# Kernel optimization log

Measured on AMD Instinct MI355X. Metric: run time of the kernel, lower is better.

Reference implementation:

```python
import jax, jax.numpy as jnp
import numpy as np
from jax import lax

B, H, W, K = 32, 384, 384, 16
SENT = H * W          # sentinel label for background / padding
THRESH = 0.75


def setup_inputs() -> dict:
    key = jax.random.key(0)
    ks = jax.random.split(key, 20)
    s = 0.1
    def n(k, shp):
        return jax.random.normal(k, shp, jnp.float32) * s
    return {
        'x1': jax.random.normal(ks[0], (B, 1, H, W), jnp.float32),
        'x2': jax.random.normal(ks[1], (B, 1, H, W), jnp.float32),
        'e1_w': n(ks[2], (16, 1, 4, 4)), 'e1_b': n(ks[3], (16,)),
        'e2_w': n(ks[4], (32, 16, 4, 4)), 'e2_b': n(ks[5], (32,)),
        'e3_w': n(ks[6], (64, 32, 4, 4)), 'e3_b': n(ks[7], (64,)),
        'd3_w': n(ks[8], (64, 32, 4, 4)), 'd3_b': n(ks[9], (32,)),
        'd2_w': n(ks[10], (64, 16, 4, 4)), 'd2_b': n(ks[11], (16,)),
        'd1_w': n(ks[12], (32, 1, 4, 4)), 'd1_b': n(ks[13], (1,)),
        'w1': n(ks[14], (32, 32)), 'b1': n(ks[15], (32,)),
        'w2': n(ks[16], (8, 32)), 'b2': n(ks[17], (8,)),
        'w3': n(ks[18], (1, 8)), 'b3': n(ks[19], (1,)),
    }


def _conv(x, w, b):  # Conv2d(k=4, s=2, p=1), torch OIHW weights
    y = lax.conv_general_dilated(x, w, (2, 2), ((1, 1), (1, 1)),
                                 dimension_numbers=('NCHW', 'OIHW', 'NCHW'))
    return y + b[None, :, None, None]


def _convT(x, w, b):  # ConvTranspose2d(k=4, s=2, p=1), torch (in,out,kh,kw) weights
    wf = jnp.flip(w, (2, 3)).transpose(1, 0, 2, 3)  # -> OIHW
    y = lax.conv_general_dilated(x, wf, (1, 1), ((2, 2), (2, 2)), lhs_dilation=(2, 2),
                                 dimension_numbers=('NCHW', 'OIHW', 'NCHW'))
    return y + b[None, :, None, None]


def _autoencoder(x, e1_w, e1_b, e2_w, e2_b, e3_w, e3_b, d3_w, d3_b, d2_w, d2_b, d1_w, d1_b):
    x1 = jax.nn.relu(_conv(x, e1_w, e1_b))
    x2 = jax.nn.relu(_conv(x1, e2_w, e2_b))
    x3 = jax.nn.relu(_conv(x2, e3_w, e3_b))
    d3 = jax.nn.relu(_convT(x3, d3_w, d3_b))
    d3 = jnp.concatenate([d3, x2], axis=1)
    d2 = jax.nn.relu(_convT(d3, d2_w, d2_b))
    d2 = jnp.concatenate([d2, x1], axis=1)
    return jax.nn.sigmoid(_convT(d2, d1_w, d1_b))


def _extract(heat):
    # 8-connected components via iterative min-label propagation, then
    # centroid -> (radius, angle deg mod 360) around image center, sorted by radius.
    fg = heat > THRESH
    idx = jnp.arange(SENT, dtype=jnp.int32).reshape(H, W)
    l0 = jnp.where(fg, idx, SENT)

    def cond(c):
        return c[1]

    def body(c):
        l, _ = c
        pooled = lax.reduce_window(l, jnp.int32(SENT), lax.min, (3, 3), (1, 1), 'SAME')
        nl = jnp.where(fg, jnp.minimum(l, pooled), SENT)
        return nl, jnp.any(nl != l)

    labels, _ = lax.while_loop(cond, body, (l0, jnp.array(True)))
    flat = labels.ravel()
    u = jnp.unique(flat, size=K + 1, fill_value=SENT)[:K]  # up to K component roots
    valid = u < SENT
    n = valid.sum()
    mask = ((flat[None, :] == u[:, None]) & valid[:, None]).astype(jnp.float32)  # (K, HW)
    cnt = jnp.maximum(mask.sum(1), 1.0)
    cols = (jnp.arange(SENT) % W).astype(jnp.float32)
    rows = (jnp.arange(SENT) // W).astype(jnp.float32)
    cx = mask @ cols / cnt
    cy = mask @ rows / cnt
    dx = cx - (W // 2)
    dy = cy - (H // 2)
    r = jnp.sqrt(dx * dx + dy * dy)
    a = jnp.rad2deg(jnp.arctan2(dy, dx)) % 360.0
    order = jnp.argsort(jnp.where(valid, r, jnp.inf))
    r = jnp.where(valid, r, 0.0)[order]
    a = jnp.where(valid, a, 0.0)[order]
    return r, a, n


def _match(r1, a1, n1, r2, a2, n2):
    # greedy nearest-radius matching of the smaller set against the larger,
    # zero padding up to K pairs; diff = (r1-r2, |sin(radians(a1-a2))|)
    swap = n1 > n2
    rA = jnp.where(swap, r2, r1); aA = jnp.where(swap, a2, a1); nA = jnp.where(swap, n2, n1)
    rB = jnp.where(swap, r1, r2); aB = jnp.where(swap, a1, a2); nB = jnp.where(swap, n1, n2)
    iota = jnp.arange(K)

    def step(used, xs):
        i, rAi, aAi = xs
        vi = i < nA
        d = jnp.where(used | (iota >= nB), jnp.inf, jnp.abs(rB - rAi))
        j = jnp.argmin(d)
        dr = rAi - rB[j]
        da = jnp.abs(jnp.sin(jnp.deg2rad(aAi - aB[j])))
        out = jnp.where(vi, jnp.stack([dr, da]), 0.0)
        used = used.at[j].set(used[j] | vi)
        return used, out

    _, ys = lax.scan(step, jnp.zeros(K, bool), (iota, rA, aA))
    return ys.ravel()  # (2K,) interleaved (dr, da) like torch flatten


def _features(x1, x2, enc):
    h1 = _autoencoder(x1, *enc)[:, 0]  # (B,H,W)
    h2 = _autoencoder(x2, *enc)[:, 0]
    r1, a1, n1 = jax.vmap(_extract)(h1)
    r2, a2, n2 = jax.vmap(_extract)(h2)
    return jax.vmap(_match)(r1, a1, n1, r2, a2, n2)  # (B, 2K)


def reference(x1, x2, e1_w, e1_b, e2_w, e2_b, e3_w, e3_b, d3_w, d3_b, d2_w, d2_b, d1_w, d1_b, w1, b1, w2, b2, w3, b3):
    enc = (e1_w, e1_b, e2_w, e2_b, e3_w, e3_b, d3_w, d3_b, d2_w, d2_b, d1_w, d1_b)
    feats = _features(x1, x2, enc)
    h = jax.nn.relu(feats @ w1.T + b1)
    h = jax.nn.relu(h @ w2.T + b2)
    return (h @ w3.T + b3)[:, 0]
```

## Files before the change

kernel.cpp:

```cpp
#include <hip/hip_runtime.h>
#include <math.h>

#define NIMG 32
#define SENTI 147456
#define CAPR 36864
#define LBG 0x7FFFFFFF

__device__ __forceinline__ int uf_load(int* P, int i) {
  return __hip_atomic_load(&P[i], __ATOMIC_RELAXED, __HIP_MEMORY_SCOPE_AGENT);
}
__device__ int uf_find(int* P, int i) {
  int p = uf_load(P, i);
  while (p != i) {
    int gp = uf_load(P, p);
    if (gp != p) atomicMin(&P[i], gp);
    i = p; p = gp;
  }
  return i;
}
__device__ void uf_union(int* P, int a, int b) {
  while (true) {
    a = uf_find(P, a); b = uf_find(P, b);
    if (a == b) return;
    if (a > b) { int t = a; a = b; b = t; }
    int old = atomicMin(&P[b], a);
    if (old == b) return;
    b = old;
  }
}

__device__ __forceinline__ int l_load(int* lab, int i) {
  return __hip_atomic_load(&lab[i], __ATOMIC_RELAXED, __HIP_MEMORY_SCOPE_WORKGROUP);
}
__device__ int l_find(int* lab, int i) {
  int p = l_load(lab, i);
  while (p != i) { int gp = l_load(lab, p); i = p; p = gp; }
  return i;
}
__device__ void l_union(int* lab, int a, int b) {
  while (true) {
    a = l_find(lab, a); b = l_find(lab, b);
    if (a == b) return;
    if (a > b) { int t = a; a = b; b = t; }
    int old = atomicMin(&lab[b], a);
    if (old == b) return;
    b = old;
  }
}

__global__ __launch_bounds__(256) void k_conv_e1(
    const float* __restrict__ x, const float* __restrict__ w,
    const float* __restrict__ bias, float* __restrict__ out)
{
  int idx = blockIdx.x * 256 + threadIdx.x;
  int ox = idx % 192; int t = idx / 192; int oy = t % 192; int img = t / 192;
  const float* xi = x + (size_t)img * 147456;
  float acc[16];
#pragma unroll
  for (int c = 0; c < 16; c++) acc[c] = bias[c];
#pragma unroll
  for (int ky = 0; ky < 4; ky++) {
    int iy = 2 * oy + ky - 1;
    if (iy < 0 || iy >= 384) continue;
    const float* row = xi + iy * 384;
#pragma unroll
    for (int kx = 0; kx < 4; kx++) {
      int ix = 2 * ox + kx - 1;
      if (ix < 0 || ix >= 384) continue;
      float v = row[ix];
#pragma unroll
      for (int c = 0; c < 16; c++) acc[c] = fmaf(v, w[c * 16 + ky * 4 + kx], acc[c]);
    }
  }
  size_t base = (size_t)img * 589824 + (size_t)oy * 192 + ox;
#pragma unroll
  for (int c = 0; c < 16; c++) out[base + (size_t)c * 36864] = fmaxf(acc[c], 0.f);
}

__global__ __launch_bounds__(256) void k_conv_e2(
    const float* __restrict__ in, const float* __restrict__ w,
    const float* __restrict__ bias, float* __restrict__ out)
{
  int idx = blockIdx.x * 256 + threadIdx.x;
  int p = idx % 48; int t = idx / 48; int oy = t % 96; int img = t / 96;
  const float* xin = in + (size_t)img * 589824;
  float accA[32], accB[32];
#pragma unroll
  for (int c = 0; c < 32; c++) { float bv = bias[c]; accA[c] = bv; accB[c] = bv; }
#pragma unroll 1
  for (int ci = 0; ci < 16; ci++) {
    const float* xc = xin + (size_t)ci * 36864;
#pragma unroll
    for (int ky = 0; ky < 4; ky++) {
      int iy = 2 * oy + ky - 1;
      float xv[6];
      if (iy >= 0 && iy < 192) {
        const float* row = xc + iy * 192;
        int c0 = 4 * p - 1;
#pragma unroll
        for (int u = 0; u < 6; u++) {
          int ix = c0 + u;
          xv[u] = (ix >= 0 && ix < 192) ? row[ix] : 0.f;
        }
      } else {
#pragma unroll
        for (int u = 0; u < 6; u++) xv[u] = 0.f;
      }
#pragma unroll
      for (int co = 0; co < 32; co++) {
        float4 wv = *(const float4*)(w + ((size_t)co * 16 + ci) * 16 + ky * 4);
        accA[co] = fmaf(xv[3], wv.w, fmaf(xv[2], wv.z, fmaf(xv[1], wv.y, fmaf(xv[0], wv.x, accA[co]))));
        accB[co] = fmaf(xv[5], wv.w, fmaf(xv[4], wv.z, fmaf(xv[3], wv.y, fmaf(xv[2], wv.x, accB[co]))));
      }
    }
  }
  size_t base = (size_t)img * 294912 + (size_t)oy * 96 + 2 * p;
#pragma unroll
  for (int co = 0; co < 32; co++) {
    float2 v; v.x = fmaxf(accA[co], 0.f); v.y = fmaxf(accB[co], 0.f);
    *(float2*)(out + base + (size_t)co * 9216) = v;
  }
}

__global__ __launch_bounds__(256) void k_conv_e3(
    const float* __restrict__ in, const float* __restrict__ w,
    const float* __restrict__ bias, float* __restrict__ out)
{
  int idx = blockIdx.x * 256 + threadIdx.x;
  int cog = blockIdx.y;
  int p = idx % 24; int t = idx / 24; int oy = t % 48; int img = t / 48;
  const float* xin = in + (size_t)img * 294912;
  float accA[16], accB[16];
#pragma unroll
  for (int c = 0; c < 16; c++) { float bv = bias[cog * 16 + c]; accA[c] = bv; accB[c] = bv; }
#pragma unroll 1
  for (int ci = 0; ci < 32; ci++) {
    const float* xc = xin + (size_t)ci * 9216;
#pragma unroll
    for (int ky = 0; ky < 4; ky++) {
      int iy = 2 * oy + ky - 1;
      float xv[6];
      if (iy >= 0 && iy < 96) {
        const float* row = xc + iy * 96;
        int c0 = 4 * p - 1;
#pragma unroll
        for (int u = 0; u < 6; u++) {
          int ix = c0 + u;
          xv[u] = (ix >= 0 && ix < 96) ? row[ix] : 0.f;
        }
      } else {
#pragma unroll
        for (int u = 0; u < 6; u++) xv[u] = 0.f;
      }
#pragma unroll
      for (int co = 0; co < 16; co++) {
        float4 wv = *(const float4*)(w + ((size_t)(cog * 16 + co) * 32 + ci) * 16 + ky * 4);
        accA[co] = fmaf(xv[3], wv.w, fmaf(xv[2], wv.z, fmaf(xv[1], wv.y, fmaf(xv[0], wv.x, accA[co]))));
        accB[co] = fmaf(xv[5], wv.w, fmaf(xv[4], wv.z, fmaf(xv[3], wv.y, fmaf(xv[2], wv.x, accB[co]))));
      }
    }
  }
  size_t base = (size_t)img * 147456 + (size_t)(cog * 16) * 2304 + (size_t)oy * 48 + 2 * p;
#pragma unroll
  for (int co = 0; co < 16; co++) {
    float2 v; v.x = fmaxf(accA[co], 0.f); v.y = fmaxf(accB[co], 0.f);
    *(float2*)(out + base + (size_t)co * 2304) = v;
  }
}

__global__ __launch_bounds__(256) void k_convt_d3(
    const float* __restrict__ in, const float* __restrict__ w,
    const float* __restrict__ bias, float* __restrict__ out)
{
  int idx = blockIdx.x * 256 + threadIdx.x;
  int p = idx % 48; int t = idx / 48; int oy = t % 96; int img = t / 96;
  int iy1 = (oy + 1) >> 1; int iy0 = iy1 - 1;
  int ky1 = (oy + 1) - 2 * iy1; int ky0 = ky1 + 2;
  bool v1 = (iy1 < 48), v0 = (iy0 >= 0);
  bool pm = (p > 0), pp = (p < 47);
  float accA[32], accB[32];
#pragma unroll
  for (int c = 0; c < 32; c++) { float bv = bias[c]; accA[c] = bv; accB[c] = bv; }
#pragma unroll 1
  for (int ci = 0; ci < 64; ci++) {
    const float* xc = in + (size_t)img * 147456 + (size_t)ci * 2304;
    const float* r1 = xc + iy1 * 48; const float* r0 = xc + iy0 * 48;
    float x1m = (v1 && pm) ? r1[p - 1] : 0.f;
    float x1c = v1 ? r1[p] : 0.f;
    float x1p = (v1 && pp) ? r1[p + 1] : 0.f;
    float x0m = (v0 && pm) ? r0[p - 1] : 0.f;
    float x0c = v0 ? r0[p] : 0.f;
    float x0p = (v0 && pp) ? r0[p + 1] : 0.f;
    const float* wb = w + (size_t)ci * 512;
#pragma unroll
    for (int co = 0; co < 32; co++) {
      float4 wv1 = *(const float4*)(wb + co * 16 + ky1 * 4);
      float4 wv0 = *(const float4*)(wb + co * 16 + ky0 * 4);
      accA[co] += x1c * wv1.y + x1m * wv1.w + x0c * wv0.y + x0m * wv0.w;
      accB[co] += x1p * wv1.x + x1c * wv1.z + x0p * wv0.x + x0c * wv0.z;
    }
  }
  size_t base = (size_t)img * 294912 + (size_t)oy * 96 + 2 * p;
#pragma unroll
  for (int co = 0; co < 32; co++) {
    float2 v; v.x = fmaxf(accA[co], 0.f); v.y = fmaxf(accB[co], 0.f);
    *(float2*)(out + base + (size_t)co * 9216) = v;
  }
}

__global__ __launch_bounds__(256) void k_convt_d2(
    const float* __restrict__ d3, const float* __restrict__ e2,
    const float* __restrict__ w, const float* __restrict__ bias,
    float* __restrict__ out)
{
  int idx = blockIdx.x * 256 + threadIdx.x;
  int pg = idx % 24; int t = idx / 24; int oy = t % 192; int img = t / 192;
  int iy1 = (oy + 1) >> 1; int iy0 = iy1 - 1;
  int ky1 = (oy + 1) - 2 * iy1; int ky0 = ky1 + 2;
  bool v1 = (iy1 < 96), v0 = (iy0 >= 0);
  int c0 = 4 * pg - 1;
  float acc[16][8];
#pragma unroll
  for (int co = 0; co < 16; co++) {
    float bv = bias[co];
#pragma unroll
    for (int j = 0; j < 8; j++) acc[co][j] = bv;
  }
  for (int half = 0; half < 2; half++) {
    const float* src = (half == 0) ? d3 : e2;
#pragma unroll 1
    for (int ci = 0; ci < 32; ci++) {
      const float* xc = src + (size_t)img * 294912 + (size_t)ci * 9216;
      const float* r1 = xc + iy1 * 96; const float* r0 = xc + iy0 * 96;
      float x1[6], x0[6];
#pragma unroll
      for (int u = 0; u < 6; u++) {
        int ix = c0 + u;
        bool cb = (ix >= 0) && (ix < 96);
        x1[u] = (v1 && cb) ? r1[ix] : 0.f;
        x0[u] = (v0 && cb) ? r0[ix] : 0.f;
      }
      const float* wb = w + (size_t)(half * 32 + ci) * 256;
#pragma unroll
      for (int co = 0; co < 16; co++) {
        float4 wv1 = *(const float4*)(wb + co * 16 + ky1 * 4);
        float4 wv0 = *(const float4*)(wb + co * 16 + ky0 * 4);
#pragma unroll
        for (int j = 0; j < 4; j++) {
          acc[co][2 * j]     += x1[j + 1] * wv1.y + x1[j] * wv1.w
                              + x0[j + 1] * wv0.y + x0[j] * wv0.w;
          acc[co][2 * j + 1] += x1[j + 2] * wv1.x + x1[j + 1] * wv1.z
                              + x0[j + 2] * wv0.x + x0[j + 1] * wv0.z;
        }
      }
    }
  }
  size_t base = (size_t)img * 589824 + (size_t)oy * 192 + 8 * pg;
#pragma unroll
  for (int co = 0; co < 16; co++) {
    float4 a, b;
    a.x = fmaxf(acc[co][0], 0.f); a.y = fmaxf(acc[co][1], 0.f);
    a.z = fmaxf(acc[co][2], 0.f); a.w = fmaxf(acc[co][3], 0.f);
    b.x = fmaxf(acc[co][4], 0.f); b.y = fmaxf(acc[co][5], 0.f);
    b.z = fmaxf(acc[co][6], 0.f); b.w = fmaxf(acc[co][7], 0.f);
    *(float4*)(out + base + (size_t)co * 36864)     = a;
    *(float4*)(out + base + (size_t)co * 36864 + 4) = b;
  }
}

__global__ __launch_bounds__(256) void k_convt_d1(
    const float* __restrict__ d2, const float* __restrict__ e1,
    const float* __restrict__ w, const float* __restrict__ bias,
    int* __restrict__ parent)
{
  int idx = blockIdx.x * 256 + threadIdx.x;
  int p = idx % 192; int t = idx / 192; int oy = t % 384; int img = t / 384;
  int iy1 = (oy + 1) >> 1; int iy0 = iy1 - 1;
  int ky1 = (oy + 1) - 2 * iy1; int ky0 = ky1 + 2;
  bool v1 = (iy1 < 192), v0 = (iy0 >= 0);
  bool pm = (p > 0), pp = (p < 191);
  float zA = bias[0], zB = bias[0];
  for (int half = 0; half < 2; half++) {
    const float* src = (half == 0) ? d2 : e1;
#pragma unroll 1
    for (int ci = 0; ci < 16; ci++) {
      const float* xc = src + (size_t)img * 589824 + (size_t)ci * 36864;
      const float* r1 = xc + iy1 * 192; const float* r0 = xc + iy0 * 192;
      float x1m = (v1 && pm) ? r1[p - 1] : 0.f;
      float x1c = v1 ? r1[p] : 0.f;
      float x1p = (v1 && pp) ? r1[p + 1] : 0.f;
      float x0m = (v0 && pm) ? r0[p - 1] : 0.f;
      float x0c = v0 ? r0[p] : 0.f;
      float x0p = (v0 && pp) ? r0[p + 1] : 0.f;
      const float* wb = w + (size_t)(half * 16 + ci) * 16;
      float4 wv1 = *(const float4*)(wb + ky1 * 4);
      float4 wv0 = *(const float4*)(wb + ky0 * 4);
      zA += x1c * wv1.y + x1m * wv1.w + x0c * wv0.y + x0m * wv0.w;
      zB += x1p * wv1.x + x1c * wv1.z + x0p * wv0.x + x0c * wv0.z;
    }
  }
  const float LN3 = 1.0986122886681098f;
  int* P = parent + (size_t)img * SENTI;
  int pixA = oy * 384 + 2 * p;
  P[pixA]     = (zA > LN3) ? pixA : SENTI;
  P[pixA + 1] = (zB > LN3) ? (pixA + 1) : SENTI;
}

__global__ __launch_bounds__(256) void k_tile_uf(int* __restrict__ parent)
{
  __shared__ int lab[1024];
  int img = blockIdx.y;
  int tile = blockIdx.x;
  int tx = tile % 12, ty = tile / 12;
  int tid = threadIdx.x;
  int* P = parent + (size_t)img * SENTI;
  int gbase = (ty * 32) * 384 + tx * 32;
  bool fg[4];
#pragma unroll
  for (int s = 0; s < 4; s++) {
    int c = tid + s * 256;
    int ly = c >> 5, lx = c & 31;
    int v = P[gbase + ly * 384 + lx];
    fg[s] = (v < SENTI);
    lab[c] = fg[s] ? c : LBG;
  }
  __syncthreads();
#pragma unroll
  for (int s = 0; s < 4; s++) {
    int c = tid + s * 256;
    if (!fg[s]) continue;
    int ly = c >> 5, lx = c & 31;
    if (lx > 0              && l_load(lab, c - 1)  != LBG) l_union(lab, c, c - 1);
    if (ly > 0) {
      if (                     l_load(lab, c - 32) != LBG) l_union(lab, c, c - 32);
      if (lx > 0            && l_load(lab, c - 33) != LBG) l_union(lab, c, c - 33);
      if (lx < 31           && l_load(lab, c - 31) != LBG) l_union(lab, c, c - 31);
    }
  }
  __syncthreads();
#pragma unroll
  for (int s = 0; s < 4; s++) {
    int c = tid + s * 256;
    if (!fg[s]) continue;
    int rc = c, q = lab[rc];
    while (q != rc) { rc = q; q = lab[rc]; }
    int rly = rc >> 5, rlx = rc & 31;
    int ly = c >> 5, lx = c & 31;
    P[gbase + ly * 384 + lx] = gbase + rly * 384 + rlx;
  }
}

__global__ __launch_bounds__(256) void k_border(int* __restrict__ parent)
{
  int idx = blockIdx.x * 256 + threadIdx.x;
  int img = idx / SENTI; int p = idx - img * SENTI;
  int* P = parent + (size_t)img * SENTI;
  int x = p % 384; int y = p / 384;
  bool bx = ((x & 31) == 0) && x > 0;
  bool by = ((y & 31) == 0) && y > 0;
  if (!bx && !by) return;
  if (P[p] >= SENTI) return;
  if (bx) {
    if (            P[p - 1]   < SENTI) uf_union(P, p, p - 1);
    if (y > 0   &&  P[p - 385] < SENTI) uf_union(P, p, p - 385);
    if (y < 383 &&  P[p + 383] < SENTI) uf_union(P, p, p + 383);
  }
  if (by) {
    if (            P[p - 384] < SENTI) uf_union(P, p, p - 384);
    if (x > 0   &&  P[p - 385] < SENTI) uf_union(P, p, p - 385);
    if (x < 383 &&  P[p - 383] < SENTI) uf_union(P, p, p - 383);
  }
}

__global__ __launch_bounds__(256) void k_flatten(
    int* __restrict__ parent, int* __restrict__ rootCnt,
    int* __restrict__ rootList, int base)
{
  __shared__ int lcnt;
  __shared__ int lbase;
  __shared__ int llist[256];
  int tid = threadIdx.x;
  if (tid == 0) lcnt = 0;
  __syncthreads();
  int idx = blockIdx.x * 256 + tid;
  int img = idx / SENTI; int p = idx - img * SENTI;
  int* P = parent + (size_t)img * SENTI;
  int v = P[p];
  if (v < SENTI) {
    int r = v, q = P[r];
    while (q != r) { r = q; q = P[r]; }
    P[p] = r;
    if (r == p) {
      int s = atomicAdd(&lcnt, 1);
      llist[s] = p;
    }
  }
  __syncthreads();
  int n = lcnt;
  if (n > 0) {
    if (tid == 0) lbase = atomicAdd(&rootCnt[base + img], n);
    __syncthreads();
    if (tid < n) rootList[(size_t)img * CAPR + lbase + tid] = llist[tid];
  }
}

__global__ __launch_bounds__(256) void k_select(
    const int* __restrict__ rootCnt, const int* __restrict__ rootList,
    int* __restrict__ U, int* __restrict__ NC, int base)
{
  int img = blockIdx.x; int tid = threadIdx.x;
  __shared__ int sv[256];
  int m = rootCnt[base + img]; if (m > CAPR) m = CAPR;
  const int* rl = rootList + (size_t)img * CAPR;
  int prev = -1;
  for (int k = 0; k < 16; k++) {
    int best = SENTI;
    for (int i = tid; i < m; i += 256) {
      int v = rl[i];
      if (v > prev && v < best) best = v;
    }
    sv[tid] = best; __syncthreads();
    for (int s = 128; s > 0; s >>= 1) {
      if (tid < s) sv[tid] = min(sv[tid], sv[tid + s]);
      __syncthreads();
    }
    int sel = sv[0];
    if (tid == 0) U[(base + img) * 16 + k] = sel;
    prev = (sel < SENTI) ? sel : 0x7FFF0000;
    __syncthreads();
  }
  if (tid == 0) NC[base + img] = (m < 16) ? m : 16;
}

__global__ __launch_bounds__(256) void k_stats(
    const int* __restrict__ parent, const int* __restrict__ U,
    int* __restrict__ CNT, float* __restrict__ SX, float* __restrict__ SY, int base)
{
  __shared__ int lc[16]; __shared__ float lx[16], ly[16];
  int tid = threadIdx.x;
  if (tid < 16) { lc[tid] = 0; lx[tid] = 0.f; ly[tid] = 0.f; }
  __syncthreads();
  int img = blockIdx.y; int g = base + img;
  int p = blockIdx.x * 256 + tid;
  int lbl = parent[(size_t)img * SENTI + p];
  if (lbl < SENTI) {
    const int* u = U + g * 16;
    int slot = -1;
#pragma unroll
    for (int s = 0; s < 16; s++) if (u[s] == lbl) slot = s;
    if (slot >= 0) {
      atomicAdd(&lc[slot], 1);
      atomicAdd(&lx[slot], (float)(p % 384));
      atomicAdd(&ly[slot], (float)(p / 384));
    }
  }
  __syncthreads();
  if (tid < 16 && lc[tid] > 0) {
    atomicAdd(&CNT[g * 16 + tid], lc[tid]);
    atomicAdd(&SX[g * 16 + tid], lx[tid]);
    atomicAdd(&SY[g * 16 + tid], ly[tid]);
  }
}

__global__ __launch_bounds__(64) void k_final(
    const int* __restrict__ U, const int* __restrict__ NC,
    const int* __restrict__ CNT, const float* __restrict__ SX,
    const float* __restrict__ SY,
    const float* __restrict__ w1, const float* __restrict__ b1,
    const float* __restrict__ w2, const float* __restrict__ b2,
    const float* __restrict__ w3, const float* __restrict__ b3,
    float* __restrict__ out)
{
  int b = threadIdx.x;
  if (b >= 32) return;
  const float INF = __builtin_inff();
  float R[2][16], A[2][16]; int N[2];
  for (int side = 0; side < 2; side++) {
    int img = b + side * 32;
    float rr[16], aa[16], key[16];
    for (int s = 0; s < 16; s++) {
      bool valid = U[img * 16 + s] < SENTI;
      float c = fmaxf((float)CNT[img * 16 + s], 1.f);
      float cx = SX[img * 16 + s] / c, cy = SY[img * 16 + s] / c;
      float dx = cx - 192.f, dy = cy - 192.f;
      rr[s] = sqrtf(dx * dx + dy * dy);
      float ang = atan2f(dy, dx) * 57.29577951308232f;
      ang = fmodf(ang, 360.f);
      if (ang < 0.f) ang += 360.f;
      aa[s] = ang;
      key[s] = valid ? rr[s] : INF;
    }
    bool taken[16];
    for (int s = 0; s < 16; s++) taken[s] = false;
    for (int k = 0; k < 16; k++) {
      int bi = -1; float bk = 0.f;
      for (int s = 0; s < 16; s++) {
        if (taken[s]) continue;
        if (bi < 0 || key[s] < bk) { bi = s; bk = key[s]; }
      }
      taken[bi] = true;
      bool val = (key[bi] < INF);
      R[side][k] = val ? rr[bi] : 0.f;
      A[side][k] = val ? aa[bi] : 0.f;
    }
    N[side] = NC[img];
  }
  int n1 = N[0], n2 = N[1];
  bool sw = n1 > n2;
  float* rA = sw ? R[1] : R[0];
  float* aA = sw ? A[1] : A[0];
  float* rB = sw ? R[0] : R[1];
  float* aB = sw ? A[0] : A[1];
  int nA = sw ? n2 : n1;
  int nB = sw ? n1 : n2;
  bool used[16];
  for (int s = 0; s < 16; s++) used[s] = false;
  float f[32];
  for (int i = 0; i < 16; i++) {
    bool vi = i < nA;
    float best = 0.f; int j = 0; bool found = false;
    for (int jj = 0; jj < 16; jj++) {
      if (used[jj] || jj >= nB) continue;
      float d = fabsf(rB[jj] - rA[i]);
      if (!found || d < best) { best = d; j = jj; found = true; }
    }
    float dr = rA[i] - rB[j];
    float da = fabsf(sinf((aA[i] - aB[j]) * 0.017453292519943295f));
    f[2 * i]     = vi ? dr : 0.f;
    f[2 * i + 1] = vi ? da : 0.f;
    if (vi) used[j] = true;
  }
  float h1[32];
  for (int jj = 0; jj < 32; jj++) {
    float s = b1[jj];
    for (int k2 = 0; k2 < 32; k2++) s += w1[jj * 32 + k2] * f[k2];
    h1[jj] = fmaxf(s, 0.f);
  }
  float h2[8];
  for (int jj = 0; jj < 8; jj++) {
    float s = b2[jj];
    for (int k2 = 0; k2 < 32; k2++) s += w2[jj * 32 + k2] * h1[k2];
    h2[jj] = fmaxf(s, 0.f);
  }
  float o = b3[0];
  for (int k2 = 0; k2 < 8; k2++) o += w3[k2] * h2[k2];
  out[b] = o;
}

extern "C" void kernel_launch(void* const* d_in, const int* in_sizes, int n_in,
                              void* d_out, int out_size, void* d_ws, size_t ws_size,
                              hipStream_t stream)
{
  (void)in_sizes; (void)n_in; (void)out_size; (void)ws_size;
  const float* x1  = (const float*)d_in[0];
  const float* x2  = (const float*)d_in[1];
  const float* e1w = (const float*)d_in[2];  const float* e1b = (const float*)d_in[3];
  const float* e2w = (const float*)d_in[4];  const float* e2b = (const float*)d_in[5];
  const float* e3w = (const float*)d_in[6];  const float* e3b = (const float*)d_in[7];
  const float* d3w = (const float*)d_in[8];  const float* d3b = (const float*)d_in[9];
  const float* d2w = (const float*)d_in[10]; const float* d2b = (const float*)d_in[11];
  const float* d1w = (const float*)d_in[12]; const float* d1b = (const float*)d_in[13];
  const float* w1  = (const float*)d_in[14]; const float* b1  = (const float*)d_in[15];
  const float* w2  = (const float*)d_in[16]; const float* b2  = (const float*)d_in[17];
  const float* w3  = (const float*)d_in[18]; const float* b3  = (const float*)d_in[19];

  char* ws = (char*)d_ws;
  float* E1 = (float*)(ws + 0);
  float* E2 = (float*)(ws + 75497472);
  float* E3 = (float*)(ws + 113246208);
  float* D3 = (float*)(ws + 132120576);
  float* D2 = (float*)(ws + 169869312);
  char* small = ws + 245366784;
  int* PARENT = (int*)E3;
  int* ROOTL  = (int*)E2;
  int*   ROOTC = (int*)(small);
  int*   U     = (int*)(small + 256);
  int*   NC    = (int*)(small + 4352);
  int*   CNT   = (int*)(small + 4608);
  float* SX    = (float*)(small + 8704);
  float* SY    = (float*)(small + 12800);

  hipMemsetAsync(ROOTC, 0, 256, stream);
  hipMemsetAsync(CNT, 0, 4096, stream);
  hipMemsetAsync(SX, 0, 4096, stream);
  hipMemsetAsync(SY, 0, 4096, stream);

  for (int pass = 0; pass < 2; pass++) {
    const float* x = (pass == 0) ? x1 : x2;
    int base = pass * 32;
    k_conv_e1<<<4608, 256, 0, stream>>>(x, e1w, e1b, E1);
    k_conv_e2<<<576, 256, 0, stream>>>(E1, e2w, e2b, E2);
    k_conv_e3<<<dim3(144, 4), 256, 0, stream>>>(E2, e3w, e3b, E3);
    k_convt_d3<<<576, 256, 0, stream>>>(E3, d3w, d3b, D3);
    k_convt_d2<<<576, 256, 0, stream>>>(D3, E2, d2w, d2b, D2);
    k_convt_d1<<<9216, 256, 0, stream>>>(D2, E1, d1w, d1b, PARENT);
    k_tile_uf<<<dim3(144, 32), 256, 0, stream>>>(PARENT);
    k_border<<<18432, 256, 0, stream>>>(PARENT);
    k_flatten<<<18432, 256, 0, stream>>>(PARENT, ROOTC, ROOTL, base);
    k_select<<<32, 256, 0, stream>>>(ROOTC, ROOTL, U, NC, base);
    k_stats<<<dim3(576, 32), 256, 0, stream>>>(PARENT, U, CNT, SX, SY, base);
  }
  k_final<<<1, 64, 0, stream>>>(U, NC, CNT, SX, SY, w1, b1, w2, b2, w3, b3, (float*)d_out);
}
```

Before: 3.271 ms.

## Retile convT d3 to 4 input columns by 8 output channels per thread

Rewrites the d3 transposed-conv kernel so each thread computes 8 output pixels (4 input columns) for an 8-channel group instead of 2 pixels for all 32 channels, with channel groups spread over blockIdx.y. This reuses each loaded weight float4 across four column positions and shares overlapping input loads. Output stores become float4 instead of float2. The thread count stays the same, but each input row is now read once per channel group, four times in total.

Result: faster. 2.857 ms (-12.6%).

```diff
diff --git a/kernel.cpp b/kernel.cpp
--- a/kernel.cpp
+++ b/kernel.cpp
@@ -173,38 +173,55 @@
     const float* __restrict__ bias, float* __restrict__ out)
 {
   int idx = blockIdx.x * 256 + threadIdx.x;
-  int p = idx % 48; int t = idx / 48; int oy = t % 96; int img = t / 96;
+  int cog = blockIdx.y;
+  int pg = idx % 12; int t = idx / 12; int oy = t % 96; int img = t / 96;
   int iy1 = (oy + 1) >> 1; int iy0 = iy1 - 1;
   int ky1 = (oy + 1) - 2 * iy1; int ky0 = ky1 + 2;
   bool v1 = (iy1 < 48), v0 = (iy0 >= 0);
-  bool pm = (p > 0), pp = (p < 47);
-  float accA[32], accB[32];
-#pragma unroll
-  for (int c = 0; c < 32; c++) { float bv = bias[c]; accA[c] = bv; accB[c] = bv; }
+  int c0 = 4 * pg - 1;
+  float acc[8][8];
+#pragma unroll
+  for (int co = 0; co < 8; co++) {
+    float bv = bias[cog * 8 + co];
+#pragma unroll
+    for (int j = 0; j < 8; j++) acc[co][j] = bv;
+  }
 #pragma unroll 1
   for (int ci = 0; ci < 64; ci++) {
     const float* xc = in + (size_t)img * 147456 + (size_t)ci * 2304;
     const float* r1 = xc + iy1 * 48; const float* r0 = xc + iy0 * 48;
-    float x1m = (v1 && pm) ? r1[p - 1] : 0.f;
-    float x1c = v1 ? r1[p] : 0.f;
-    float x1p = (v1 && pp) ? r1[p + 1] : 0.f;
-    float x0m = (v0 && pm) ? r0[p - 1] : 0.f;
-    float x0c = v0 ? r0[p] : 0.f;
-    float x0p = (v0 && pp) ? r0[p + 1] : 0.f;
+    float x1[6], x0[6];
+#pragma unroll
+    for (int u = 0; u < 6; u++) {
+      int ix = c0 + u;
+      bool cb = (ix >= 0) && (ix < 48);
+      x1[u] = (v1 && cb) ? r1[ix] : 0.f;
+      x0[u] = (v0 && cb) ? r0[ix] : 0.f;
+    }
     const float* wb = w + (size_t)ci * 512;
 #pragma unroll
-    for (int co = 0; co < 32; co++) {
-      float4 wv1 = *(const float4*)(wb + co * 16 + ky1 * 4);
-      float4 wv0 = *(const float4*)(wb + co * 16 + ky0 * 4);
-      accA[co] += x1c * wv1.y + x1m * wv1.w + x0c * wv0.y + x0m * wv0.w;
-      accB[co] += x1p * wv1.x + x1c * wv1.z + x0p * wv0.x + x0c * wv0.z;
-    }
-  }
-  size_t base = (size_t)img * 294912 + (size_t)oy * 96 + 2 * p;
-#pragma unroll
-  for (int co = 0; co < 32; co++) {
-    float2 v; v.x = fmaxf(accA[co], 0.f); v.y = fmaxf(accB[co], 0.f);
-    *(float2*)(out + base + (size_t)co * 9216) = v;
+    for (int co = 0; co < 8; co++) {
+      float4 wv1 = *(const float4*)(wb + (cog * 8 + co) * 16 + ky1 * 4);
+      float4 wv0 = *(const float4*)(wb + (cog * 8 + co) * 16 + ky0 * 4);
+#pragma unroll
+      for (int j = 0; j < 4; j++) {
+        acc[co][2 * j]     += x1[j + 1] * wv1.y + x1[j] * wv1.w
+                            + x0[j + 1] * wv0.y + x0[j] * wv0.w;
+        acc[co][2 * j + 1] += x1[j + 2] * wv1.x + x1[j + 1] * wv1.z
+                            + x0[j + 2] * wv0.x + x0[j + 1] * wv0.z;
+      }
+    }
+  }
+  size_t base = (size_t)img * 294912 + (size_t)(cog * 8) * 9216 + (size_t)oy * 96 + 8 * pg;
+#pragma unroll
+  for (int co = 0; co < 8; co++) {
+    float4 a, b;
+    a.x = fmaxf(acc[co][0], 0.f); a.y = fmaxf(acc[co][1], 0.f);
+    a.z = fmaxf(acc[co][2], 0.f); a.w = fmaxf(acc[co][3], 0.f);
+    b.x = fmaxf(acc[co][4], 0.f); b.y = fmaxf(acc[co][5], 0.f);
+    b.z = fmaxf(acc[co][6], 0.f); b.w = fmaxf(acc[co][7], 0.f);
+    *(float4*)(out + base + (size_t)co * 9216)     = a;
+    *(float4*)(out + base + (size_t)co * 9216 + 4) = b;
   }
 }
 
@@ -591,7 +608,7 @@
     k_conv_e1<<<4608, 256, 0, stream>>>(x, e1w, e1b, E1);
     k_conv_e2<<<576, 256, 0, stream>>>(E1, e2w, e2b, E2);
     k_conv_e3<<<dim3(144, 4), 256, 0, stream>>>(E2, e3w, e3b, E3);
-    k_convt_d3<<<576, 256, 0, stream>>>(E3, d3w, d3b, D3);
+    k_convt_d3<<<dim3(144, 4), 256, 0, stream>>>(E3, d3w, d3b, D3);
     k_convt_d2<<<576, 256, 0, stream>>>(D3, E2, d2w, d2b, D2);
     k_convt_d1<<<9216, 256, 0, stream>>>(D2, E1, d1w, d1b, PARENT);
     k_tile_uf<<<dim3(144, 32), 256, 0, stream>>>(PARENT);
```
